# Kernel tuning notes

Hardware: AMD Instinct MI355X
Metric: run time of the kernel (lower is better)

Reference implementation:

```python
import jax, jax.numpy as jnp
import numpy as np

N_NODES = 200000
N_EDGES = 600000
N_GRAPHS = 4000
EMB = 128
LAYERS = 5
TASKS = 128
ATOM_FEATS, ATOM_VOCAB = 9, 64
BOND_FEATS, BOND_VOCAB = 3, 8
BN_EPS = 1e-5


def setup_inputs() -> dict:
    key = jax.random.key(0)
    ks = jax.random.split(key, 16)
    x = jax.random.randint(ks[0], (N_NODES, ATOM_FEATS), 0, ATOM_VOCAB)
    edge_index = jax.random.randint(ks[1], (2, N_EDGES), 0, N_NODES)
    edge_attr = jax.random.randint(ks[2], (N_EDGES, BOND_FEATS), 0, BOND_VOCAB)
    batch = jnp.sort(jax.random.randint(ks[3], (N_NODES,), 0, N_GRAPHS))
    s = 1.0 / np.sqrt(EMB)
    atom_emb = jax.random.normal(ks[4], (ATOM_FEATS, ATOM_VOCAB, EMB), jnp.float32) * s
    bond_emb = jax.random.normal(ks[5], (LAYERS, BOND_FEATS, BOND_VOCAB, EMB), jnp.float32) * s
    W = jax.random.normal(ks[6], (LAYERS, EMB, EMB), jnp.float32) * s
    b = jax.random.normal(ks[7], (LAYERS, EMB), jnp.float32) * 0.01
    root = jax.random.normal(ks[8], (LAYERS, EMB), jnp.float32) * s
    bn_mean = jax.random.normal(ks[9], (LAYERS, EMB), jnp.float32) * 0.1
    bn_var = jax.random.uniform(ks[10], (LAYERS, EMB), jnp.float32, 0.5, 1.5)
    bn_gamma = jax.random.uniform(ks[11], (LAYERS, EMB), jnp.float32, 0.5, 1.5)
    bn_beta = jax.random.normal(ks[12], (LAYERS, EMB), jnp.float32) * 0.1
    headW = jax.random.normal(ks[13], (EMB, TASKS), jnp.float32) * s
    headb = jnp.zeros((TASKS,), jnp.float32)
    return {"x": x, "edge_index": edge_index, "edge_attr": edge_attr, "batch": batch,
            "atom_emb": atom_emb, "bond_emb": bond_emb, "W": W, "b": b, "root": root,
            "bn_mean": bn_mean, "bn_var": bn_var, "bn_gamma": bn_gamma, "bn_beta": bn_beta,
            "headW": headW, "headb": headb}


def _gcn_forward(x, edge_index, edge_attr, batch, atom_emb, bond_emb, W, b, root,
                 bn_mean, bn_var, bn_gamma, bn_beta, headW, headb):
    src, dst = edge_index[0], edge_index[1]
    # AtomEncoder: sum of per-feature embeddings  -> [N, EMB]
    h = jnp.sum(jnp.take_along_axis(atom_emb, x.T[:, :, None], axis=1).squeeze(2), axis=0) \
        if False else sum(atom_emb[f][x[:, f]] for f in range(ATOM_FEATS))
    # degree of source nodes (+1 self loop), as in OGB GCNConv
    deg = jnp.zeros((N_NODES,), h.dtype).at[src].add(1.0) + 1.0
    dinv = deg ** -0.5
    norm = dinv[src] * dinv[dst]  # [E]
    for l in range(LAYERS):
        xl = h @ W[l] + b[l]
        edge_emb = sum(bond_emb[l, f][edge_attr[:, f]] for f in range(BOND_FEATS))  # [E, EMB]
        msg = norm[:, None] * jax.nn.relu(xl[src] + edge_emb)
        agg = jax.ops.segment_sum(msg, dst, num_segments=N_NODES)
        h = agg + jax.nn.relu(xl + root[l]) / deg[:, None]
        # BatchNorm1d (eval mode: running stats)
        h = (h - bn_mean[l]) * (bn_gamma[l] / jnp.sqrt(bn_var[l] + BN_EPS)) + bn_beta[l]
        if l != LAYERS - 1:
            h = jax.nn.relu(h)
        # dropout is identity in eval mode
    # global_add_pool over graphs
    hg = jax.ops.segment_sum(h, batch, num_segments=N_GRAPHS)
    return hg @ headW + headb


def reference(x, edge_index, edge_attr, batch, atom_emb, bond_emb, W, b, root,
              bn_mean, bn_var, bn_gamma, bn_beta, headW, headb):
    return _gcn_forward(x, edge_index, edge_attr, batch, atom_emb, bond_emb, W, b, root,
                        bn_mean, bn_var, bn_gamma, bn_beta, headW, headb)
```

## Files before the change

### kernel.cpp

```cpp
#include <hip/hip_runtime.h>
#include <hip/hip_bf16.h>

#define N_NODES 200000
#define N_EDGES 600000
#define N_GRAPHS 4000
#define EMB 128
#define LAYERS 5
#define BN_EPS 1e-5f

#define SCAN_CHUNK 2048
#define N_CHUNKS ((N_NODES + SCAN_CHUNK - 1) / SCAN_CHUNK)

typedef __attribute__((ext_vector_type(8))) short short8;
typedef __attribute__((ext_vector_type(8))) unsigned short ushort8v;
typedef __attribute__((ext_vector_type(4))) float float4v;

__device__ __forceinline__ void bf16split(float f, unsigned short& hi, unsigned short& lo) {
    unsigned u = __float_as_uint(f);
    hi = (unsigned short)(u >> 16);
    float hf = __uint_as_float((unsigned)hi << 16);
    lo = (unsigned short)(__float_as_uint(f - hf) >> 16);
}

__device__ __forceinline__ unsigned short f2bf_rne(float f) {
    unsigned u = __float_as_uint(f);
    u += 0x7FFF + ((u >> 16) & 1);
    return (unsigned short)(u >> 16);
}
__device__ __forceinline__ float bf2f(unsigned short h) {
    return __uint_as_float((unsigned)h << 16);
}

#define CNT_BLOCKS 2344
#define WP_BASE   CNT_BLOCKS
#define WP_BLOCKS 320
#define CB_BASE   (WP_BASE + WP_BLOCKS)
#define CB_BLOCKS 1280
#define BN_BASE   (CB_BASE + CB_BLOCKS)
#define BN_BLOCKS 3
#define GB_BASE   (BN_BASE + BN_BLOCKS)
#define GB_BLOCKS 16
#define PREP_BLOCKS (GB_BASE + GB_BLOCKS)

__global__ __launch_bounds__(256) void prep_all(
    const int* __restrict__ ei_src, const int* __restrict__ ei_dst,
    int* __restrict__ dsrc, int* __restrict__ ddst,
    const float* __restrict__ W, unsigned short* __restrict__ whi,
    unsigned short* __restrict__ wlo,
    const float* __restrict__ bemb, float* __restrict__ combo,
    const float* __restrict__ mean, const float* __restrict__ var,
    const float* __restrict__ gamma, const float* __restrict__ beta,
    float* __restrict__ S, float* __restrict__ T,
    const int* __restrict__ batch, int* __restrict__ gptr) {
    const int b = blockIdx.x, tid = threadIdx.x;
    if (b < CNT_BLOCKS) {
        const int e = b * 256 + tid;
        if (e < N_EDGES) {
            atomicAdd(&dsrc[ei_src[e]], 1);
            atomicAdd(&ddst[ei_dst[e]], 1);
        }
    } else if (b < CB_BASE) {
        const int idx = (b - WP_BASE) * 256 + tid;
        const int l = idx >> 14, rem = idx & 16383;
        const int k = rem >> 7, n = rem & 127;
        unsigned short hi, lo;
        bf16split(W[idx], hi, lo);
        const int off = (l << 14) + ((((k >> 5) * 8 + (n >> 4)) * 64
                        + ((k >> 3) & 3) * 16 + (n & 15)) << 3) + (k & 7);
        whi[off] = hi;
        wlo[off] = lo;
    } else if (b < BN_BASE) {
        const int idx = (b - CB_BASE) * 256 + tid;
        const int l = idx >> 16;
        const int c = (idx >> 7) & 511;
        const int ch = idx & 127;
        const int a0 = c & 7, a1 = (c >> 3) & 7, a2 = c >> 6;
        combo[(size_t)(l * 512 + c) * EMB + ch] =
            bemb[(size_t)((l * 3 + 0) * 8 + a0) * EMB + ch] +
            bemb[(size_t)((l * 3 + 1) * 8 + a1) * EMB + ch] +
            bemb[(size_t)((l * 3 + 2) * 8 + a2) * EMB + ch];
    } else if (b < GB_BASE) {
        const int i = (b - BN_BASE) * 256 + tid;
        if (i < LAYERS * EMB) {
            float s = gamma[i] / sqrtf(var[i] + BN_EPS);
            S[i] = s;
            T[i] = beta[i] - mean[i] * s;
        }
    } else {
        const int g = (b - GB_BASE) * 256 + tid;
        if (g > N_GRAPHS) return;
        if (g == N_GRAPHS) { gptr[g] = N_NODES; return; }
        int lo = 0, hi = N_NODES;
        while (lo < hi) {
            int mid = (lo + hi) >> 1;
            if (batch[mid] < g) lo = mid + 1; else hi = mid;
        }
        gptr[g] = lo;
    }
}

__global__ __launch_bounds__(256) void scan1(const int* __restrict__ deg, int* __restrict__ partial) {
    __shared__ int sd[256];
    const int base = blockIdx.x * SCAN_CHUNK + threadIdx.x * 8;
    int s = 0;
#pragma unroll
    for (int i = 0; i < 8; ++i) { int idx = base + i; s += (idx < N_NODES) ? deg[idx] : 0; }
    sd[threadIdx.x] = s; __syncthreads();
    for (int off = 128; off > 0; off >>= 1) {
        if (threadIdx.x < off) sd[threadIdx.x] += sd[threadIdx.x + off];
        __syncthreads();
    }
    if (threadIdx.x == 0) partial[blockIdx.x] = sd[0];
}

__global__ __launch_bounds__(256) void scan3(const int* __restrict__ deg,
                                             const int* __restrict__ partial,
                                             int* __restrict__ rowptr) {
    __shared__ int sd[256];
    __shared__ int base_off;
    const int tid = threadIdx.x;
    if (tid == 0) {
        int acc = 0;
        for (int i = 0; i < (int)blockIdx.x; ++i) acc += partial[i];
        base_off = acc;
    }
    const int base = blockIdx.x * SCAN_CHUNK + tid * 8;
    int loc[8]; int s = 0;
#pragma unroll
    for (int i = 0; i < 8; ++i) { int idx = base + i; loc[i] = (idx < N_NODES) ? deg[idx] : 0; s += loc[i]; }
    sd[tid] = s; __syncthreads();
    for (int off = 1; off < 256; off <<= 1) {
        int v = (tid >= off) ? sd[tid - off] : 0;
        __syncthreads();
        sd[tid] += v;
        __syncthreads();
    }
    int excl = base_off + sd[tid] - s;
#pragma unroll
    for (int i = 0; i < 8; ++i) {
        int idx = base + i;
        if (idx < N_NODES) { rowptr[idx] = excl; excl += loc[i]; }
    }
    if (blockIdx.x == 0 && tid == 0) rowptr[N_NODES] = N_EDGES;
}

__global__ void scatter_k(const int* __restrict__ srcs, const int* __restrict__ dsts,
                          const int* __restrict__ eattr, const int* __restrict__ dsrc,
                          const int* __restrict__ rowptr, int* __restrict__ fill,
                          int* __restrict__ epk, float* __restrict__ enrm) {
    int e = blockIdx.x * blockDim.x + threadIdx.x;
    if (e >= N_EDGES) return;
    const int s = srcs[e];
    const int d = dsts[e];
    const int pos = rowptr[d] + atomicAdd(&fill[d], 1);
    const int c = eattr[e * 3] | (eattr[e * 3 + 1] << 3) | (eattr[e * 3 + 2] << 6);
    epk[pos] = s | (c << 18);
    enrm[pos] = rsqrtf((float)(dsrc[s] + 1) * (float)(dsrc[d] + 1));
}

__device__ __forceinline__ void mfma_tile64(
    unsigned short (*AhAl)[64][136],
    const short8* __restrict__ Bh, const short8* __restrict__ Bl,
    const float* __restrict__ bias, unsigned short* __restrict__ XLout,
    size_t rows, int tid) {
    const int wave = tid >> 6;
    const int lane = tid & 63;
    const int quad = lane >> 4;
    const int n15  = lane & 15;
    const int rt   = wave & 3;
    const int cp   = wave >> 2;
    const int arow = rt * 16 + n15;

    float4v acc0 = (float4v)(0.f);
    float4v acc1 = (float4v)(0.f);
#pragma unroll
    for (int ks = 0; ks < 4; ++ks) {
        const int k0 = ks * 32 + quad * 8;
        const short8 ah = *(const short8*)&AhAl[0][arow][k0];
        const short8 al = *(const short8*)&AhAl[1][arow][k0];
        const short8 bh0 = Bh[(ks * 8 + cp * 2 + 0) * 64 + lane];
        const short8 bl0 = Bl[(ks * 8 + cp * 2 + 0) * 64 + lane];
        const short8 bh1 = Bh[(ks * 8 + cp * 2 + 1) * 64 + lane];
        const short8 bl1 = Bl[(ks * 8 + cp * 2 + 1) * 64 + lane];
        acc0 = __builtin_amdgcn_mfma_f32_16x16x32_bf16(ah, bh0, acc0, 0, 0, 0);
        acc0 = __builtin_amdgcn_mfma_f32_16x16x32_bf16(ah, bl0, acc0, 0, 0, 0);
        acc0 = __builtin_amdgcn_mfma_f32_16x16x32_bf16(al, bh0, acc0, 0, 0, 0);
        acc1 = __builtin_amdgcn_mfma_f32_16x16x32_bf16(ah, bh1, acc1, 0, 0, 0);
        acc1 = __builtin_amdgcn_mfma_f32_16x16x32_bf16(ah, bl1, acc1, 0, 0, 0);
        acc1 = __builtin_amdgcn_mfma_f32_16x16x32_bf16(al, bh1, acc1, 0, 0, 0);
    }

    const size_t rowBase = rows + rt * 16 + quad * 4;
    const int col0 = (cp * 2 + 0) * 16 + n15;
    const int col1 = (cp * 2 + 1) * 16 + n15;
    const float bc0 = bias[col0];
    const float bc1 = bias[col1];
#pragma unroll
    for (int r = 0; r < 4; ++r) {
        XLout[(rowBase + r) * EMB + col0] = f2bf_rne(acc0[r] + bc0);
        XLout[(rowBase + r) * EMB + col1] = f2bf_rne(acc1[r] + bc1);
    }
}

__global__ __launch_bounds__(1024, 8) void enc_gemm(
    const int* __restrict__ x, const float* __restrict__ aemb,
    const unsigned short* __restrict__ whi, const unsigned short* __restrict__ wlo,
    const float* __restrict__ bias, unsigned short* __restrict__ XL) {
    __shared__ unsigned short AhAl[2][64][136];
    const int tid = threadIdx.x;
    const int q = tid & 15, qw = tid >> 4;
    const int c0 = q * 8;
    const size_t rows = (size_t)blockIdx.x * 64;

    {
        const size_t n = rows + qw;
        float4 a0 = make_float4(0.f, 0.f, 0.f, 0.f), a1 = a0;
#pragma unroll
        for (int ff = 0; ff < 9; ++ff) {
            const int v = x[n * 9 + ff];
            const float4 e0 = *(const float4*)&aemb[(size_t)(ff * 64 + v) * EMB + c0];
            const float4 e1 = *(const float4*)&aemb[(size_t)(ff * 64 + v) * EMB + c0 + 4];
            a0.x += e0.x; a0.y += e0.y; a0.z += e0.z; a0.w += e0.w;
            a1.x += e1.x; a1.y += e1.y; a1.z += e1.z; a1.w += e1.w;
        }
        ushort4 hi, lo;
        bf16split(a0.x, hi.x, lo.x); bf16split(a0.y, hi.y, lo.y);
        bf16split(a0.z, hi.z, lo.z); bf16split(a0.w, hi.w, lo.w);
        *(ushort4*)&AhAl[0][qw][c0] = hi;
        *(ushort4*)&AhAl[1][qw][c0] = lo;
        bf16split(a1.x, hi.x, lo.x); bf16split(a1.y, hi.y, lo.y);
        bf16split(a1.z, hi.z, lo.z); bf16split(a1.w, hi.w, lo.w);
        *(ushort4*)&AhAl[0][qw][c0 + 4] = hi;
        *(ushort4*)&AhAl[1][qw][c0 + 4] = lo;
    }
    __syncthreads();
    mfma_tile64(AhAl, (const short8*)whi, (const short8*)wlo, bias, XL, rows, tid);
}

__global__ __launch_bounds__(1024, 8) void gather_gemm(
    const int* __restrict__ rowptr, const int* __restrict__ epk,
    const float* __restrict__ enrm, const float* __restrict__ combo,
    const float* __restrict__ root, const int* __restrict__ dsrc,
    const float* __restrict__ bnS, const float* __restrict__ bnT,
    const unsigned short* __restrict__ whi, const unsigned short* __restrict__ wlo,
    const float* __restrict__ bias,
    const unsigned short* __restrict__ XLin, unsigned short* __restrict__ XLout) {
    __shared__ unsigned short AhAl[2][64][136];
    const int tid = threadIdx.x;
    const int q = tid & 15, qw = tid >> 4;
    const int c0 = q * 8;
    const size_t rows = (size_t)blockIdx.x * 64;

    {
        const size_t n = rows + qw;
        const float4 r40 = *(const float4*)&root[c0];
        const float4 r41 = *(const float4*)&root[c0 + 4];
        const float4 s40 = *(const float4*)&bnS[c0];
        const float4 s41 = *(const float4*)&bnS[c0 + 4];
        const float4 t40 = *(const float4*)&bnT[c0];
        const float4 t41 = *(const float4*)&bnT[c0 + 4];
        const float dinv = 1.0f / (float)(dsrc[n] + 1);
        const ushort8v xn = *(const ushort8v*)&XLin[n * EMB + c0];
        float4 a0, a1;
        a0.x = fmaxf(bf2f(xn[0]) + r40.x, 0.f) * dinv;
        a0.y = fmaxf(bf2f(xn[1]) + r40.y, 0.f) * dinv;
        a0.z = fmaxf(bf2f(xn[2]) + r40.z, 0.f) * dinv;
        a0.w = fmaxf(bf2f(xn[3]) + r40.w, 0.f) * dinv;
        a1.x = fmaxf(bf2f(xn[4]) + r41.x, 0.f) * dinv;
        a1.y = fmaxf(bf2f(xn[5]) + r41.y, 0.f) * dinv;
        a1.z = fmaxf(bf2f(xn[6]) + r41.z, 0.f) * dinv;
        a1.w = fmaxf(bf2f(xn[7]) + r41.w, 0.f) * dinv;

        const int beg = rowptr[n], end = rowptr[n + 1];
        int pk = 0; float wgt = 0.f;
        if (beg < end) { pk = epk[beg]; wgt = enrm[beg]; }
        for (int e = beg; e < end; ++e) {
            const int pk_c = pk; const float w_c = wgt;
            if (e + 1 < end) { pk = epk[e + 1]; wgt = enrm[e + 1]; }
            const size_t sb = (size_t)(pk_c & 0x3FFFF) * EMB + c0;
            const size_t cbx = (size_t)(pk_c >> 18) * EMB + c0;
            const ushort8v xv = *(const ushort8v*)&XLin[sb];
            const float4 cb0 = *(const float4*)&combo[cbx];
            const float4 cb1 = *(const float4*)&combo[cbx + 4];
            a0.x += fmaxf(bf2f(xv[0]) + cb0.x, 0.f) * w_c;
            a0.y += fmaxf(bf2f(xv[1]) + cb0.y, 0.f) * w_c;
            a0.z += fmaxf(bf2f(xv[2]) + cb0.z, 0.f) * w_c;
            a0.w += fmaxf(bf2f(xv[3]) + cb0.w, 0.f) * w_c;
            a1.x += fmaxf(bf2f(xv[4]) + cb1.x, 0.f) * w_c;
            a1.y += fmaxf(bf2f(xv[5]) + cb1.y, 0.f) * w_c;
            a1.z += fmaxf(bf2f(xv[6]) + cb1.z, 0.f) * w_c;
            a1.w += fmaxf(bf2f(xv[7]) + cb1.w, 0.f) * w_c;
        }
        float4 h0, h1;
        h0.x = fmaxf(fmaf(a0.x, s40.x, t40.x), 0.f);
        h0.y = fmaxf(fmaf(a0.y, s40.y, t40.y), 0.f);
        h0.z = fmaxf(fmaf(a0.z, s40.z, t40.z), 0.f);
        h0.w = fmaxf(fmaf(a0.w, s40.w, t40.w), 0.f);
        h1.x = fmaxf(fmaf(a1.x, s41.x, t41.x), 0.f);
        h1.y = fmaxf(fmaf(a1.y, s41.y, t41.y), 0.f);
        h1.z = fmaxf(fmaf(a1.z, s41.z, t41.z), 0.f);
        h1.w = fmaxf(fmaf(a1.w, s41.w, t41.w), 0.f);
        ushort4 hi, lo;
        bf16split(h0.x, hi.x, lo.x); bf16split(h0.y, hi.y, lo.y);
        bf16split(h0.z, hi.z, lo.z); bf16split(h0.w, hi.w, lo.w);
        *(ushort4*)&AhAl[0][qw][c0] = hi;
        *(ushort4*)&AhAl[1][qw][c0] = lo;
        bf16split(h1.x, hi.x, lo.x); bf16split(h1.y, hi.y, lo.y);
        bf16split(h1.z, hi.z, lo.z); bf16split(h1.w, hi.w, lo.w);
        *(ushort4*)&AhAl[0][qw][c0 + 4] = hi;
        *(ushort4*)&AhAl[1][qw][c0 + 4] = lo;
    }
    __syncthreads();
    mfma_tile64(AhAl, (const short8*)whi, (const short8*)wlo, bias, XLout, rows, tid);
}

__global__ __launch_bounds__(512) void gather_pool_head(
    const int* __restrict__ rowptr, const int* __restrict__ epk,
    const float* __restrict__ enrm, const float* __restrict__ combo,
    const float* __restrict__ root, const int* __restrict__ dsrc,
    const float* __restrict__ S4, const float* __restrict__ T4,
    const int* __restrict__ gptr, const unsigned short* __restrict__ XLin,
    const float* __restrict__ HW, const float* __restrict__ hb,
    float* __restrict__ OUT) {
    __shared__ float red[32][EMB];
    __shared__ float hr[EMB];
    const int gph = blockIdx.x;
    const int q = threadIdx.x & 15, qw = threadIdx.x >> 4;
    const int c0 = q * 8;
    const int nbeg = gptr[gph], nend = gptr[gph + 1];

    const float4 r40 = *(const float4*)&root[c0];
    const float4 r41 = *(const float4*)&root[c0 + 4];
    const float4 s40 = *(const float4*)&S4[c0];
    const float4 s41 = *(const float4*)&S4[c0 + 4];
    const float4 t40 = *(const float4*)&T4[c0];
    const float4 t41 = *(const float4*)&T4[c0 + 4];

    float4 seg0 = make_float4(0.f, 0.f, 0.f, 0.f), seg1 = seg0;
    for (int n = nbeg + qw; n < nend; n += 32) {
        const float dinv = 1.0f / (float)(dsrc[n] + 1);
        const ushort8v xn = *(const ushort8v*)&XLin[(size_t)n * EMB + c0];
        float4 a0, a1;
        a0.x = fmaxf(bf2f(xn[0]) + r40.x, 0.f) * dinv;
        a0.y = fmaxf(bf2f(xn[1]) + r40.y, 0.f) * dinv;
        a0.z = fmaxf(bf2f(xn[2]) + r40.z, 0.f) * dinv;
        a0.w = fmaxf(bf2f(xn[3]) + r40.w, 0.f) * dinv;
        a1.x = fmaxf(bf2f(xn[4]) + r41.x, 0.f) * dinv;
        a1.y = fmaxf(bf2f(xn[5]) + r41.y, 0.f) * dinv;
        a1.z = fmaxf(bf2f(xn[6]) + r41.z, 0.f) * dinv;
        a1.w = fmaxf(bf2f(xn[7]) + r41.w, 0.f) * dinv;
        const int beg = rowptr[n], end = rowptr[n + 1];
        int pk = 0; float wgt = 0.f;
        if (beg < end) { pk = epk[beg]; wgt = enrm[beg]; }
        for (int e = beg; e < end; ++e) {
            const int pk_c = pk; const float w_c = wgt;
            if (e + 1 < end) { pk = epk[e + 1]; wgt = enrm[e + 1]; }
            const size_t sb = (size_t)(pk_c & 0x3FFFF) * EMB + c0;
            const size_t cbx = (size_t)(pk_c >> 18) * EMB + c0;
            const ushort8v xv = *(const ushort8v*)&XLin[sb];
            const float4 cb0 = *(const float4*)&combo[cbx];
            const float4 cb1 = *(const float4*)&combo[cbx + 4];
            a0.x += fmaxf(bf2f(xv[0]) + cb0.x, 0.f) * w_c;
            a0.y += fmaxf(bf2f(xv[1]) + cb0.y, 0.f) * w_c;
            a0.z += fmaxf(bf2f(xv[2]) + cb0.z, 0.f) * w_c;
            a0.w += fmaxf(bf2f(xv[3]) + cb0.w, 0.f) * w_c;
            a1.x += fmaxf(bf2f(xv[4]) + cb1.x, 0.f) * w_c;
            a1.y += fmaxf(bf2f(xv[5]) + cb1.y, 0.f) * w_c;
            a1.z += fmaxf(bf2f(xv[6]) + cb1.z, 0.f) * w_c;
            a1.w += fmaxf(bf2f(xv[7]) + cb1.w, 0.f) * w_c;
        }
        seg0.x += fmaf(a0.x, s40.x, t40.x);
        seg0.y += fmaf(a0.y, s40.y, t40.y);
        seg0.z += fmaf(a0.z, s40.z, t40.z);
        seg0.w += fmaf(a0.w, s40.w, t40.w);
        seg1.x += fmaf(a1.x, s41.x, t41.x);
        seg1.y += fmaf(a1.y, s41.y, t41.y);
        seg1.z += fmaf(a1.z, s41.z, t41.z);
        seg1.w += fmaf(a1.w, s41.w, t41.w);
    }
    *(float4*)&red[qw][c0] = seg0;
    *(float4*)&red[qw][c0 + 4] = seg1;
    __syncthreads();

    const int t = threadIdx.x;
    if (t < EMB) {
        float v = 0.f;
#pragma unroll
        for (int r = 0; r < 32; ++r) v += red[r][t];
        hr[t] = v;
    }
    __syncthreads();
    if (t < EMB) {
        float o = hb[t];
#pragma unroll 8
        for (int k = 0; k < EMB; ++k) o = fmaf(hr[k], HW[(size_t)k * EMB + t], o);
        OUT[(size_t)gph * EMB + t] = o;
    }
}

extern "C" void kernel_launch(void* const* d_in, const int* in_sizes, int n_in,
                              void* d_out, int out_size, void* d_ws, size_t ws_size,
                              hipStream_t stream) {
    const int*   x     = (const int*)d_in[0];
    const int*   ei    = (const int*)d_in[1];
    const int*   ea    = (const int*)d_in[2];
    const int*   batch = (const int*)d_in[3];
    const float* aemb  = (const float*)d_in[4];
    const float* bemb  = (const float*)d_in[5];
    const float* W     = (const float*)d_in[6];
    const float* b     = (const float*)d_in[7];
    const float* root  = (const float*)d_in[8];
    const float* bnm   = (const float*)d_in[9];
    const float* bnv   = (const float*)d_in[10];
    const float* bng   = (const float*)d_in[11];
    const float* bnb   = (const float*)d_in[12];
    const float* hW    = (const float*)d_in[13];
    const float* hb    = (const float*)d_in[14];
    float* out = (float*)d_out;

    const size_t NF = (size_t)N_NODES * EMB;
    const size_t n_float = NF + (size_t)LAYERS * 512 * EMB
                         + 2 * LAYERS * EMB + N_EDGES
                         + 2 * ((size_t)LAYERS * 16384 / 2 + 64);
    const size_t n_int   = 3 * (size_t)N_NODES + (N_NODES + 4) + 128
                         + (N_GRAPHS + 4) + N_EDGES;
    const size_t need = (n_float + n_int) * sizeof(float);
    if (ws_size < need) return;

    float* f     = (float*)d_ws;
    unsigned short* bufA = (unsigned short*)f; f += NF / 2;
    unsigned short* bufB = (unsigned short*)f; f += NF / 2;
    float* combo = f;                          f += (size_t)LAYERS * 512 * EMB;
    float* S     = f;                          f += LAYERS * EMB;
    float* T     = f;                          f += LAYERS * EMB;
    float* enrm  = f;                          f += N_EDGES;
    unsigned short* whi = (unsigned short*)f;  f += (size_t)LAYERS * 16384 / 2 + 64;
    unsigned short* wlo = (unsigned short*)f;  f += (size_t)LAYERS * 16384 / 2 + 64;
    int*   ip    = (int*)f;
    int*   dsrc    = ip;                       ip += N_NODES;
    int*   ddst    = ip;                       ip += N_NODES;
    int*   fill    = ip;                       ip += N_NODES;
    int*   rowptr  = ip;                       ip += N_NODES + 4;
    int*   partial = ip;                       ip += 128;
    int*   gptr    = ip;                       ip += N_GRAPHS + 4;
    int*   epk     = ip;                       ip += N_EDGES;

    hipMemsetAsync(dsrc, 0, 3 * (size_t)N_NODES * sizeof(int), stream);

    prep_all<<<PREP_BLOCKS, 256, 0, stream>>>(
        ei, ei + N_EDGES, dsrc, ddst, W, whi, wlo, bemb, combo,
        bnm, bnv, bng, bnb, S, T, batch, gptr);
    scan1<<<N_CHUNKS, 256, 0, stream>>>(ddst, partial);
    scan3<<<N_CHUNKS, 256, 0, stream>>>(ddst, partial, rowptr);
    scatter_k<<<(N_EDGES + 255) / 256, 256, 0, stream>>>(ei, ei + N_EDGES, ea, dsrc,
                                                         rowptr, fill, epk, enrm);

    enc_gemm<<<N_NODES / 64, 1024, 0, stream>>>(x, aemb, whi, wlo, b, bufA);

    unsigned short* in    = bufA;
    unsigned short* other = bufB;
    for (int l = 0; l < 4; ++l) {
        gather_gemm<<<N_NODES / 64, 1024, 0, stream>>>(
            rowptr, epk, enrm, combo + (size_t)l * 512 * EMB, root + l * EMB, dsrc,
            S + l * EMB, T + l * EMB,
            whi + (size_t)(l + 1) * 16384, wlo + (size_t)(l + 1) * 16384,
            b + (l + 1) * EMB, in, other);
        unsigned short* t0 = in; in = other; other = t0;
    }

    gather_pool_head<<<N_GRAPHS, 512, 0, stream>>>(
        rowptr, epk, enrm, combo + (size_t)4 * 512 * EMB, root + 4 * EMB, dsrc,
        S + 4 * EMB, T + 4 * EMB, gptr, in, hW, hb, out);
}
```

Measured before the change: 627.4 us.

## Balance edge aggregation across block via edge-parallel LDS atomics

After: 2.034 ms. 3.24x slower.

```diff
diff --git a/kernel.cpp b/kernel.cpp
--- a/kernel.cpp
+++ b/kernel.cpp
@@ -147,7 +147,8 @@
 __global__ void scatter_k(const int* __restrict__ srcs, const int* __restrict__ dsts,
                           const int* __restrict__ eattr, const int* __restrict__ dsrc,
                           const int* __restrict__ rowptr, int* __restrict__ fill,
-                          int* __restrict__ epk, float* __restrict__ enrm) {
+                          int* __restrict__ epk, float* __restrict__ enrm,
+                          unsigned char* __restrict__ dloc) {
     int e = blockIdx.x * blockDim.x + threadIdx.x;
     if (e >= N_EDGES) return;
     const int s = srcs[e];
@@ -156,6 +157,7 @@
     const int c = eattr[e * 3] | (eattr[e * 3 + 1] << 3) | (eattr[e * 3 + 2] << 6);
     epk[pos] = s | (c << 18);
     enrm[pos] = rsqrtf((float)(dsrc[s] + 1) * (float)(dsrc[d] + 1));
+    dloc[pos] = (unsigned char)(d & 63);
 }
 
 __device__ __forceinline__ void mfma_tile64(
@@ -239,12 +241,14 @@
 
 __global__ __launch_bounds__(1024, 8) void gather_gemm(
     const int* __restrict__ rowptr, const int* __restrict__ epk,
-    const float* __restrict__ enrm, const float* __restrict__ combo,
+    const float* __restrict__ enrm, const unsigned char* __restrict__ dloc,
+    const float* __restrict__ combo,
     const float* __restrict__ root, const int* __restrict__ dsrc,
     const float* __restrict__ bnS, const float* __restrict__ bnT,
     const unsigned short* __restrict__ whi, const unsigned short* __restrict__ wlo,
     const float* __restrict__ bias,
     const unsigned short* __restrict__ XLin, unsigned short* __restrict__ XLout) {
+    __shared__ float Acc[64][132];
     __shared__ unsigned short AhAl[2][64][136];
     const int tid = threadIdx.x;
     const int q = tid & 15, qw = tid >> 4;
@@ -253,60 +257,66 @@
 
     {
         const size_t n = rows + qw;
+        const float dinv = 1.0f / (float)(dsrc[n] + 1);
+        const ushort8v xn = *(const ushort8v*)&XLin[n * EMB + c0];
         const float4 r40 = *(const float4*)&root[c0];
         const float4 r41 = *(const float4*)&root[c0 + 4];
+        Acc[qw][c0 + 0] = fmaxf(bf2f(xn[0]) + r40.x, 0.f) * dinv;
+        Acc[qw][c0 + 1] = fmaxf(bf2f(xn[1]) + r40.y, 0.f) * dinv;
+        Acc[qw][c0 + 2] = fmaxf(bf2f(xn[2]) + r40.z, 0.f) * dinv;
+        Acc[qw][c0 + 3] = fmaxf(bf2f(xn[3]) + r40.w, 0.f) * dinv;
+        Acc[qw][c0 + 4] = fmaxf(bf2f(xn[4]) + r41.x, 0.f) * dinv;
+        Acc[qw][c0 + 5] = fmaxf(bf2f(xn[5]) + r41.y, 0.f) * dinv;
+        Acc[qw][c0 + 6] = fmaxf(bf2f(xn[6]) + r41.z, 0.f) * dinv;
+        Acc[qw][c0 + 7] = fmaxf(bf2f(xn[7]) + r41.w, 0.f) * dinv;
+    }
+    __syncthreads();
+
+    {
+        const int ebeg = rowptr[rows];
+        const int eend = rowptr[rows + 64];
+        for (int i = ebeg + qw; i < eend; i += 64) {
+            const int pk = epk[i];
+            const float w = enrm[i];
+            const int dl = dloc[i];
+            const size_t sb = (size_t)(pk & 0x3FFFF) * EMB + c0;
+            const size_t cbx = (size_t)(pk >> 18) * EMB + c0;
+            const ushort8v xv = *(const ushort8v*)&XLin[sb];
+            const float4 cb0 = *(const float4*)&combo[cbx];
+            const float4 cb1 = *(const float4*)&combo[cbx + 4];
+            atomicAdd(&Acc[dl][c0 + 0], fmaxf(bf2f(xv[0]) + cb0.x, 0.f) * w);
+            atomicAdd(&Acc[dl][c0 + 1], fmaxf(bf2f(xv[1]) + cb0.y, 0.f) * w);
+            atomicAdd(&Acc[dl][c0 + 2], fmaxf(bf2f(xv[2]) + cb0.z, 0.f) * w);
+            atomicAdd(&Acc[dl][c0 + 3], fmaxf(bf2f(xv[3]) + cb0.w, 0.f) * w);
+            atomicAdd(&Acc[dl][c0 + 4], fmaxf(bf2f(xv[4]) + cb1.x, 0.f) * w);
+            atomicAdd(&Acc[dl][c0 + 5], fmaxf(bf2f(xv[5]) + cb1.y, 0.f) * w);
+            atomicAdd(&Acc[dl][c0 + 6], fmaxf(bf2f(xv[6]) + cb1.z, 0.f) * w);
+            atomicAdd(&Acc[dl][c0 + 7], fmaxf(bf2f(xv[7]) + cb1.w, 0.f) * w);
+        }
+    }
+    __syncthreads();
+
+    {
         const float4 s40 = *(const float4*)&bnS[c0];
         const float4 s41 = *(const float4*)&bnS[c0 + 4];
         const float4 t40 = *(const float4*)&bnT[c0];
         const float4 t41 = *(const float4*)&bnT[c0 + 4];
-        const float dinv = 1.0f / (float)(dsrc[n] + 1);
-        const ushort8v xn = *(const ushort8v*)&XLin[n * EMB + c0];
-        float4 a0, a1;
-        a0.x = fmaxf(bf2f(xn[0]) + r40.x, 0.f) * dinv;
-        a0.y = fmaxf(bf2f(xn[1]) + r40.y, 0.f) * dinv;
-        a0.z = fmaxf(bf2f(xn[2]) + r40.z, 0.f) * dinv;
-        a0.w = fmaxf(bf2f(xn[3]) + r40.w, 0.f) * dinv;
-        a1.x = fmaxf(bf2f(xn[4]) + r41.x, 0.f) * dinv;
-        a1.y = fmaxf(bf2f(xn[5]) + r41.y, 0.f) * dinv;
-        a1.z = fmaxf(bf2f(xn[6]) + r41.z, 0.f) * dinv;
-        a1.w = fmaxf(bf2f(xn[7]) + r41.w, 0.f) * dinv;
-
-        const int beg = rowptr[n], end = rowptr[n + 1];
-        int pk = 0; float wgt = 0.f;
-        if (beg < end) { pk = epk[beg]; wgt = enrm[beg]; }
-        for (int e = beg; e < end; ++e) {
-            const int pk_c = pk; const float w_c = wgt;
-            if (e + 1 < end) { pk = epk[e + 1]; wgt = enrm[e + 1]; }
-            const size_t sb = (size_t)(pk_c & 0x3FFFF) * EMB + c0;
-            const size_t cbx = (size_t)(pk_c >> 18) * EMB + c0;
-            const ushort8v xv = *(const ushort8v*)&XLin[sb];
-            const float4 cb0 = *(const float4*)&combo[cbx];
-            const float4 cb1 = *(const float4*)&combo[cbx + 4];
-            a0.x += fmaxf(bf2f(xv[0]) + cb0.x, 0.f) * w_c;
-            a0.y += fmaxf(bf2f(xv[1]) + cb0.y, 0.f) * w_c;
-            a0.z += fmaxf(bf2f(xv[2]) + cb0.z, 0.f) * w_c;
-            a0.w += fmaxf(bf2f(xv[3]) + cb0.w, 0.f) * w_c;
-            a1.x += fmaxf(bf2f(xv[4]) + cb1.x, 0.f) * w_c;
-            a1.y += fmaxf(bf2f(xv[5]) + cb1.y, 0.f) * w_c;
-            a1.z += fmaxf(bf2f(xv[6]) + cb1.z, 0.f) * w_c;
-            a1.w += fmaxf(bf2f(xv[7]) + cb1.w, 0.f) * w_c;
-        }
-        float4 h0, h1;
-        h0.x = fmaxf(fmaf(a0.x, s40.x, t40.x), 0.f);
-        h0.y = fmaxf(fmaf(a0.y, s40.y, t40.y), 0.f);
-        h0.z = fmaxf(fmaf(a0.z, s40.z, t40.z), 0.f);
-        h0.w = fmaxf(fmaf(a0.w, s40.w, t40.w), 0.f);
-        h1.x = fmaxf(fmaf(a1.x, s41.x, t41.x), 0.f);
-        h1.y = fmaxf(fmaf(a1.y, s41.y, t41.y), 0.f);
-        h1.z = fmaxf(fmaf(a1.z, s41.z, t41.z), 0.f);
-        h1.w = fmaxf(fmaf(a1.w, s41.w, t41.w), 0.f);
+        float h[8];
+        h[0] = fmaxf(fmaf(Acc[qw][c0 + 0], s40.x, t40.x), 0.f);
+        h[1] = fmaxf(fmaf(Acc[qw][c0 + 1], s40.y, t40.y), 0.f);
+        h[2] = fmaxf(fmaf(Acc[qw][c0 + 2], s40.z, t40.z), 0.f);
+        h[3] = fmaxf(fmaf(Acc[qw][c0 + 3], s40.w, t40.w), 0.f);
+        h[4] = fmaxf(fmaf(Acc[qw][c0 + 4], s41.x, t41.x), 0.f);
+        h[5] = fmaxf(fmaf(Acc[qw][c0 + 5], s41.y, t41.y), 0.f);
+        h[6] = fmaxf(fmaf(Acc[qw][c0 + 6], s41.z, t41.z), 0.f);
+        h[7] = fmaxf(fmaf(Acc[qw][c0 + 7], s41.w, t41.w), 0.f);
         ushort4 hi, lo;
-        bf16split(h0.x, hi.x, lo.x); bf16split(h0.y, hi.y, lo.y);
-        bf16split(h0.z, hi.z, lo.z); bf16split(h0.w, hi.w, lo.w);
+        bf16split(h[0], hi.x, lo.x); bf16split(h[1], hi.y, lo.y);
+        bf16split(h[2], hi.z, lo.z); bf16split(h[3], hi.w, lo.w);
         *(ushort4*)&AhAl[0][qw][c0] = hi;
         *(ushort4*)&AhAl[1][qw][c0] = lo;
-        bf16split(h1.x, hi.x, lo.x); bf16split(h1.y, hi.y, lo.y);
-        bf16split(h1.z, hi.z, lo.z); bf16split(h1.w, hi.w, lo.w);
+        bf16split(h[4], hi.x, lo.x); bf16split(h[5], hi.y, lo.y);
+        bf16split(h[6], hi.z, lo.z); bf16split(h[7], hi.w, lo.w);
         *(ushort4*)&AhAl[0][qw][c0 + 4] = hi;
         *(ushort4*)&AhAl[1][qw][c0 + 4] = lo;
     }
@@ -328,55 +338,40 @@
     const int q = threadIdx.x & 15, qw = threadIdx.x >> 4;
     const int c0 = q * 8;
     const int nbeg = gptr[gph], nend = gptr[gph + 1];
+    const int ebeg = rowptr[nbeg], eend = rowptr[nend];
 
     const float4 r40 = *(const float4*)&root[c0];
     const float4 r41 = *(const float4*)&root[c0 + 4];
-    const float4 s40 = *(const float4*)&S4[c0];
-    const float4 s41 = *(const float4*)&S4[c0 + 4];
-    const float4 t40 = *(const float4*)&T4[c0];
-    const float4 t41 = *(const float4*)&T4[c0 + 4];
 
     float4 seg0 = make_float4(0.f, 0.f, 0.f, 0.f), seg1 = seg0;
     for (int n = nbeg + qw; n < nend; n += 32) {
         const float dinv = 1.0f / (float)(dsrc[n] + 1);
         const ushort8v xn = *(const ushort8v*)&XLin[(size_t)n * EMB + c0];
-        float4 a0, a1;
-        a0.x = fmaxf(bf2f(xn[0]) + r40.x, 0.f) * dinv;
-        a0.y = fmaxf(bf2f(xn[1]) + r40.y, 0.f) * dinv;
-        a0.z = fmaxf(bf2f(xn[2]) + r40.z, 0.f) * dinv;
-        a0.w = fmaxf(bf2f(xn[3]) + r40.w, 0.f) * dinv;
-        a1.x = fmaxf(bf2f(xn[4]) + r41.x, 0.f) * dinv;
-        a1.y = fmaxf(bf2f(xn[5]) + r41.y, 0.f) * dinv;
-        a1.z = fmaxf(bf2f(xn[6]) + r41.z, 0.f) * dinv;
-        a1.w = fmaxf(bf2f(xn[7]) + r41.w, 0.f) * dinv;
-        const int beg = rowptr[n], end = rowptr[n + 1];
-        int pk = 0; float wgt = 0.f;
-        if (beg < end) { pk = epk[beg]; wgt = enrm[beg]; }
-        for (int e = beg; e < end; ++e) {
-            const int pk_c = pk; const float w_c = wgt;
-            if (e + 1 < end) { pk = epk[e + 1]; wgt = enrm[e + 1]; }
-            const size_t sb = (size_t)(pk_c & 0x3FFFF) * EMB + c0;
-            const size_t cbx = (size_t)(pk_c >> 18) * EMB + c0;
-            const ushort8v xv = *(const ushort8v*)&XLin[sb];
-            const float4 cb0 = *(const float4*)&combo[cbx];
-            const float4 cb1 = *(const float4*)&combo[cbx + 4];
-            a0.x += fmaxf(bf2f(xv[0]) + cb0.x, 0.f) * w_c;
-            a0.y += fmaxf(bf2f(xv[1]) + cb0.y, 0.f) * w_c;
-            a0.z += fmaxf(bf2f(xv[2]) + cb0.z, 0.f) * w_c;
-            a0.w += fmaxf(bf2f(xv[3]) + cb0.w, 0.f) * w_c;
-            a1.x += fmaxf(bf2f(xv[4]) + cb1.x, 0.f) * w_c;
-            a1.y += fmaxf(bf2f(xv[5]) + cb1.y, 0.f) * w_c;
-            a1.z += fmaxf(bf2f(xv[6]) + cb1.z, 0.f) * w_c;
-            a1.w += fmaxf(bf2f(xv[7]) + cb1.w, 0.f) * w_c;
-        }
-        seg0.x += fmaf(a0.x, s40.x, t40.x);
-        seg0.y += fmaf(a0.y, s40.y, t40.y);
-        seg0.z += fmaf(a0.z, s40.z, t40.z);
-        seg0.w += fmaf(a0.w, s40.w, t40.w);
-        seg1.x += fmaf(a1.x, s41.x, t41.x);
-        seg1.y += fmaf(a1.y, s41.y, t41.y);
-        seg1.z += fmaf(a1.z, s41.z, t41.z);
-        seg1.w += fmaf(a1.w, s41.w, t41.w);
+        seg0.x += fmaxf(bf2f(xn[0]) + r40.x, 0.f) * dinv;
+        seg0.y += fmaxf(bf2f(xn[1]) + r40.y, 0.f) * dinv;
+        seg0.z += fmaxf(bf2f(xn[2]) + r40.z, 0.f) * dinv;
+        seg0.w += fmaxf(bf2f(xn[3]) + r40.w, 0.f) * dinv;
+        seg1.x += fmaxf(bf2f(xn[4]) + r41.x, 0.f) * dinv;
+        seg1.y += fmaxf(bf2f(xn[5]) + r41.y, 0.f) * dinv;
+        seg1.z += fmaxf(bf2f(xn[6]) + r41.z, 0.f) * dinv;
+        seg1.w += fmaxf(bf2f(xn[7]) + r41.w, 0.f) * dinv;
+    }
+    for (int i = ebeg + qw; i < eend; i += 32) {
+        const int pk = epk[i];
+        const float w = enrm[i];
+        const size_t sb = (size_t)(pk & 0x3FFFF) * EMB + c0;
+        const size_t cbx = (size_t)(pk >> 18) * EMB + c0;
+        const ushort8v xv = *(const ushort8v*)&XLin[sb];
+        const float4 cb0 = *(const float4*)&combo[cbx];
+        const float4 cb1 = *(const float4*)&combo[cbx + 4];
+        seg0.x += fmaxf(bf2f(xv[0]) + cb0.x, 0.f) * w;
+        seg0.y += fmaxf(bf2f(xv[1]) + cb0.y, 0.f) * w;
+        seg0.z += fmaxf(bf2f(xv[2]) + cb0.z, 0.f) * w;
+        seg0.w += fmaxf(bf2f(xv[3]) + cb0.w, 0.f) * w;
+        seg1.x += fmaxf(bf2f(xv[4]) + cb1.x, 0.f) * w;
+        seg1.y += fmaxf(bf2f(xv[5]) + cb1.y, 0.f) * w;
+        seg1.z += fmaxf(bf2f(xv[6]) + cb1.z, 0.f) * w;
+        seg1.w += fmaxf(bf2f(xv[7]) + cb1.w, 0.f) * w;
     }
     *(float4*)&red[qw][c0] = seg0;
     *(float4*)&red[qw][c0 + 4] = seg1;
@@ -387,7 +382,7 @@
         float v = 0.f;
 #pragma unroll
         for (int r = 0; r < 32; ++r) v += red[r][t];
-        hr[t] = v;
+        hr[t] = fmaf(v, S4[t], T4[t] * (float)(nend - nbeg));
     }
     __syncthreads();
     if (t < EMB) {
@@ -423,7 +418,8 @@
                          + 2 * LAYERS * EMB + N_EDGES
                          + 2 * ((size_t)LAYERS * 16384 / 2 + 64);
     const size_t n_int   = 3 * (size_t)N_NODES + (N_NODES + 4) + 128
-                         + (N_GRAPHS + 4) + N_EDGES;
+                         + (N_GRAPHS + 4) + N_EDGES
+                         + (N_EDGES / 4 + 16);
     const size_t need = (n_float + n_int) * sizeof(float);
     if (ws_size < need) return;
 
@@ -444,6 +440,7 @@
     int*   partial = ip;                       ip += 128;
     int*   gptr    = ip;                       ip += N_GRAPHS + 4;
     int*   epk     = ip;                       ip += N_EDGES;
+    unsigned char* dloc = (unsigned char*)ip;
 
     hipMemsetAsync(dsrc, 0, 3 * (size_t)N_NODES * sizeof(int), stream);
 
@@ -453,7 +450,7 @@
     scan1<<<N_CHUNKS, 256, 0, stream>>>(ddst, partial);
     scan3<<<N_CHUNKS, 256, 0, stream>>>(ddst, partial, rowptr);
     scatter_k<<<(N_EDGES + 255) / 256, 256, 0, stream>>>(ei, ei + N_EDGES, ea, dsrc,
-                                                         rowptr, fill, epk, enrm);
+                                                         rowptr, fill, epk, enrm, dloc);
 
     enc_gemm<<<N_NODES / 64, 1024, 0, stream>>>(x, aemb, whi, wlo, b, bufA);
 
@@ -461,7 +458,7 @@
     unsigned short* other = bufB;
     for (int l = 0; l < 4; ++l) {
         gather_gemm<<<N_NODES / 64, 1024, 0, stream>>>(
-            rowptr, epk, enrm, combo + (size_t)l * 512 * EMB, root + l * EMB, dsrc,
+            rowptr, epk, enrm, dloc, combo + (size_t)l * 512 * EMB, root + l * EMB, dsrc,
             S + l * EMB, T + l * EMB,
             whi + (size_t)(l + 1) * 16384, wlo + (size_t)(l + 1) * 16384,
             b + (l + 1) * EMB, in, other);
```
